# Performance work log

Measured on AMD Instinct MI355X. Metric: run time of the kernel, lower is better.

Reference implementation:

```python
import jax, jax.numpy as jnp
import numpy as np

B, S, H = 8, 512, 768
NH, DH = 12, 64
I = 3072
E = 8
TOPK = 2
EPS = 1e-12


def _ln(x, g, b):
    m = jnp.mean(x, axis=-1, keepdims=True)
    v = jnp.mean(jnp.square(x - m), axis=-1, keepdims=True)
    return (x - m) * jax.lax.rsqrt(v + EPS) * g + b


def setup_inputs() -> dict:
    key = jax.random.key(0)
    ks = jax.random.split(key, 20)
    s_h = 1.0 / np.sqrt(H)
    s_i = 1.0 / np.sqrt(I)
    inp = {
        "hidden_states": jax.random.normal(ks[0], (B, S, H), jnp.float32),
        "Wq": jax.random.normal(ks[1], (H, H), jnp.float32) * s_h,
        "bq": jnp.zeros((H,), jnp.float32),
        "Wk": jax.random.normal(ks[2], (H, H), jnp.float32) * s_h,
        "bk": jnp.zeros((H,), jnp.float32),
        "Wv": jax.random.normal(ks[3], (H, H), jnp.float32) * s_h,
        "bv": jnp.zeros((H,), jnp.float32),
        "Wo": jax.random.normal(ks[4], (H, H), jnp.float32) * s_h,
        "bo": jnp.zeros((H,), jnp.float32),
        "ln_attn_g": jnp.ones((H,), jnp.float32),
        "ln_attn_b": jnp.zeros((H,), jnp.float32),
        "ln_ffn_g": jnp.ones((H,), jnp.float32),
        "ln_ffn_b": jnp.zeros((H,), jnp.float32),
        "Wr": jax.random.normal(ks[5], (H, E), jnp.float32) * s_h,
        "br": jnp.zeros((E,), jnp.float32),
        "W_up": jax.random.normal(ks[6], (E, H, I), jnp.float32) * s_h,
        "b_up": jnp.zeros((E, I), jnp.float32),
        "W_new": jax.random.normal(ks[7], (E, H, I), jnp.float32) * s_h,
        "b_new": jnp.zeros((E, I), jnp.float32),
        "W_down": jax.random.normal(ks[8], (E, I, H), jnp.float32) * s_i,
        "b_down": jnp.zeros((E, H), jnp.float32),
    }
    return inp


def reference(hidden_states, Wq, bq, Wk, bk, Wv, bv, Wo, bo,
              ln_attn_g, ln_attn_b, ln_ffn_g, ln_ffn_b,
              Wr, br, W_up, b_up, W_new, b_new, W_down, b_down):
    x = hidden_states
    # --- BertSelfAttention ---
    q = (x @ Wq + bq).reshape(B, S, NH, DH).transpose(0, 2, 1, 3)
    k = (x @ Wk + bk).reshape(B, S, NH, DH).transpose(0, 2, 1, 3)
    v = (x @ Wv + bv).reshape(B, S, NH, DH).transpose(0, 2, 1, 3)
    scores = jnp.einsum("bhqd,bhkd->bhqk", q, k) / np.sqrt(DH)
    probs = jax.nn.softmax(scores, axis=-1)
    ctx = jnp.einsum("bhqk,bhkd->bhqd", probs, v)
    ctx = ctx.transpose(0, 2, 1, 3).reshape(B, S, H)
    # --- BertSelfOutput: dense + residual + LayerNorm ---
    attention_output = _ln(ctx @ Wo + bo + x, ln_attn_g, ln_attn_b)
    # --- feed_forward_chunk: LayerNorm then token top-k MoE ---
    xl = _ln(attention_output, ln_ffn_g, ln_ffn_b)
    router_logits = xl @ Wr + br                      # [B,S,E]
    router_probs = jax.nn.softmax(router_logits, axis=-1)
    topw, topi = jax.lax.top_k(router_probs, TOPK)    # [B,S,K]
    topw = topw / jnp.sum(topw, axis=-1, keepdims=True)
    gates = jnp.sum(jax.nn.one_hot(topi, E, dtype=xl.dtype) * topw[..., None], axis=-2)  # [B,S,E]
    # --- experts (BertExpert: gelu(up(x)) * new(x) -> down), dense over E ---
    up = jax.nn.gelu(jnp.einsum("bsh,ehi->ebsi", xl, W_up) + b_up[:, None, None, :], approximate=False)
    gate_h = jnp.einsum("bsh,ehi->ebsi", xl, W_new) + b_new[:, None, None, :]
    y = jnp.einsum("ebsi,eih->ebsh", up * gate_h, W_down) + b_down[:, None, None, :]
    moe_out = jnp.einsum("ebsh,bse->bsh", y, gates)
    layer_output = moe_out + attention_output
    return layer_output, router_logits
```

## Files before the change

kernel.cpp:

```cpp
#include <hip/hip_runtime.h>
#include <hip/hip_bf16.h>
#include <cmath>


constexpr int cB = 8, cS = 512, cH = 768, cNH = 12, cDH = 64, cI = 3072, cE = 8;
constexpr int cT = cB * cS;
constexpr size_t TH = (size_t)cT * cH;

typedef __hip_bfloat16 bf16;
typedef __attribute__((ext_vector_type(8))) short s8v;
typedef __attribute__((ext_vector_type(4))) float f4v;

constexpr size_t SZ_WEXP     = (size_t)cE * cI * cH / 2;
constexpr size_t OFF_WUP_T   = 0;
constexpr size_t OFF_WNEW_T  = OFF_WUP_T + SZ_WEXP;
constexpr size_t OFF_WDOWN_T = OFF_WNEW_T + SZ_WEXP;
constexpr size_t OFF_QKV     = OFF_WDOWN_T + SZ_WEXP;
constexpr size_t OFF_CTX     = OFF_QKV + 4 * TH;
constexpr size_t OFF_XLB     = OFF_CTX + TH;
constexpr size_t OFF_WGT     = OFF_XLB + TH / 2;
constexpr size_t OFF_COUNTS  = OFF_WGT + 2 * cT;
constexpr size_t OFF_LISTS   = OFF_COUNTS + 16;

__device__ __forceinline__ void glds16(const void* g, void* l) {
    __builtin_amdgcn_global_load_lds(
        (const __attribute__((address_space(1))) unsigned int*)g,
        (__attribute__((address_space(3))) unsigned int*)l, 16, 0, 0);
}

__global__ void init_counts_kernel(int* __restrict__ counts) {
    if (threadIdx.x < cE) counts[threadIdx.x] = 0;
}

__global__ __launch_bounds__(256) void transpose_bf16_kernel(
    const float* __restrict__ src, bf16* __restrict__ dst, int R, int C) {
    __shared__ float tile[64][65];
    const size_t zb = (size_t)blockIdx.z * R * C;
    const int r0 = blockIdx.y * 64, c0 = blockIdx.x * 64;
    const int t = threadIdx.x;
    const int lr = t >> 4, lc = (t & 15) * 4;
#pragma unroll
    for (int i = 0; i < 4; ++i) {
        float4 v = *(const float4*)(src + zb + (size_t)(r0 + lr + i * 16) * C + c0 + lc);
        tile[lr + i * 16][lc + 0] = v.x; tile[lr + i * 16][lc + 1] = v.y;
        tile[lr + i * 16][lc + 2] = v.z; tile[lr + i * 16][lc + 3] = v.w;
    }
    __syncthreads();
#pragma unroll
    for (int i = 0; i < 4; ++i) {
        int cr = lr + i * 16;
        bf16 o[4];
#pragma unroll
        for (int j = 0; j < 4; ++j) o[j] = (bf16)tile[lc + j][cr];
        *(uint2*)(dst + zb + (size_t)(c0 + cr) * R + r0 + lc) = *(uint2*)o;
    }
}

__device__ __forceinline__ void gemm_body128(
    const float* __restrict__ A, const float* __restrict__ B,
    const float* __restrict__ bias, float* __restrict__ C,
    int N, int K, int m0, int n0, int kbeg, int kend, bool addb) {
    __shared__ float As[16 * 132];
    __shared__ float Bs[16 * 128];
    const int t = threadIdx.x;
    const int tx = t & 15, ty = t >> 4;
    const int ar = t >> 2, ac = (t & 3) * 4;
    const float* gB0 = B + (size_t)(kbeg + (t >> 5)) * N + n0 + (t & 31) * 4;
    float* dB0 = Bs + t * 4;
    float acc[8][8] = {};
    for (int k0 = kbeg; k0 < kend; k0 += 16) {
        float4 a0 = *(const float4*)(A + (size_t)(m0 + ar) * K + k0 + ac);
        float4 a1 = *(const float4*)(A + (size_t)(m0 + ar + 64) * K + k0 + ac);
        glds16(gB0, dB0);
        glds16(gB0 + (size_t)8 * N, dB0 + 1024);
        As[(ac + 0) * 132 + ar] = a0.x; As[(ac + 1) * 132 + ar] = a0.y;
        As[(ac + 2) * 132 + ar] = a0.z; As[(ac + 3) * 132 + ar] = a0.w;
        As[(ac + 0) * 132 + ar + 64] = a1.x; As[(ac + 1) * 132 + ar + 64] = a1.y;
        As[(ac + 2) * 132 + ar + 64] = a1.z; As[(ac + 3) * 132 + ar + 64] = a1.w;
        __syncthreads();
#pragma unroll
        for (int kk = 0; kk < 16; ++kk) {
            float a[8], b[8];
            *(float4*)&a[0] = *(const float4*)&As[kk * 132 + ty * 8];
            *(float4*)&a[4] = *(const float4*)&As[kk * 132 + ty * 8 + 4];
            *(float4*)&b[0] = *(const float4*)&Bs[kk * 128 + tx * 4];
            *(float4*)&b[4] = *(const float4*)&Bs[kk * 128 + tx * 4 + 64];
#pragma unroll
            for (int i = 0; i < 8; ++i)
#pragma unroll
                for (int j = 0; j < 8; ++j) acc[i][j] += a[i] * b[j];
        }
        __syncthreads();
        gB0 += (size_t)16 * N;
    }
#pragma unroll
    for (int i = 0; i < 8; ++i) {
        int m = m0 + ty * 8 + i;
        float4 o0, o1;
        o0.x = acc[i][0]; o0.y = acc[i][1]; o0.z = acc[i][2]; o0.w = acc[i][3];
        o1.x = acc[i][4]; o1.y = acc[i][5]; o1.z = acc[i][6]; o1.w = acc[i][7];
        if (addb) {
            o0.x += bias[n0 + tx * 4 + 0]; o0.y += bias[n0 + tx * 4 + 1];
            o0.z += bias[n0 + tx * 4 + 2]; o0.w += bias[n0 + tx * 4 + 3];
            o1.x += bias[n0 + 64 + tx * 4 + 0]; o1.y += bias[n0 + 64 + tx * 4 + 1];
            o1.z += bias[n0 + 64 + tx * 4 + 2]; o1.w += bias[n0 + 64 + tx * 4 + 3];
        }
        *(float4*)(C + (size_t)m * N + n0 + tx * 4) = o0;
        *(float4*)(C + (size_t)m * N + n0 + 64 + tx * 4) = o1;
    }
}

__global__ __launch_bounds__(256) void gemm_qkv_kernel(
    const float* __restrict__ A,
    const float* __restrict__ Wq, const float* __restrict__ Wk,
    const float* __restrict__ Wv,
    const float* __restrict__ bq, const float* __restrict__ bk,
    const float* __restrict__ bv,
    float* __restrict__ q0, float* __restrict__ k0, float* __restrict__ v0,
    float* __restrict__ q1, float* __restrict__ k1, float* __restrict__ v1) {
    const int z = blockIdx.z;
    const int p = z >> 1, ks = z & 1;
    const float* B = (p == 0) ? Wq : (p == 1) ? Wk : Wv;
    const float* bias = (p == 0) ? bq : (p == 1) ? bk : bv;
    float* C = (p == 0) ? (ks ? q1 : q0)
             : (p == 1) ? (ks ? k1 : k0)
                        : (ks ? v1 : v0);
    gemm_body128(A, B, bias, C, cH, cH, blockIdx.y * 128, blockIdx.x * 128,
                 ks * 384, ks * 384 + 384, ks == 0);
}

__global__ __launch_bounds__(256) void reduce_qkv_kernel(
    float* __restrict__ dst2, const float* __restrict__ src2,
    float* __restrict__ v0, const float* __restrict__ v1) {
    const size_t n2 = 2 * TH / 4, n3 = 3 * TH / 4;
    for (size_t i = (size_t)blockIdx.x * 256 + threadIdx.x; i < n3;
         i += (size_t)gridDim.x * 256) {
        if (i < n2) {
            float4 a = ((const float4*)dst2)[i];
            float4 b = ((const float4*)src2)[i];
            a.x += b.x; a.y += b.y; a.z += b.z; a.w += b.w;
            ((float4*)dst2)[i] = a;
        } else {
            size_t j = i - n2;
            float4 a = ((const float4*)v0)[j];
            float4 b = ((const float4*)v1)[j];
            a.x += b.x; a.y += b.y; a.z += b.z; a.w += b.w;
            ((float4*)v0)[j] = a;
        }
    }
}

__global__ __launch_bounds__(256) void gemm_wo_kernel(
    const float* __restrict__ A, const float* __restrict__ W,
    const float* __restrict__ bias,
    float* __restrict__ p0, float* __restrict__ p1,
    float* __restrict__ p2, float* __restrict__ p3) {
    const int ks = blockIdx.z;
    float* C = (ks == 0) ? p0 : (ks == 1) ? p1 : (ks == 2) ? p2 : p3;
    gemm_body128(A, W, bias, C, cH, cH, blockIdx.y * 128, blockIdx.x * 128,
                 ks * 192, ks * 192 + 192, ks == 0);
}

__global__ __launch_bounds__(256) void attn_kernel(
    const float* __restrict__ q, const float* __restrict__ k,
    const float* __restrict__ v, float* __restrict__ ctx) {
    __shared__ float sQ[64][68];
    __shared__ float sKV[64][68];
    __shared__ float sS[64][68];
    __shared__ float sM[64], sL[64], sAl[64];
    const int q0 = blockIdx.x * 64, h = blockIdx.y, b = blockIdx.z;
    const int t = threadIdx.x;
    const int lr = t >> 2, lq = (t & 3) * 16;
    {
        const float* gq = q + (size_t)(b * cS + q0 + lr) * cH + h * cDH + lq;
#pragma unroll
        for (int j = 0; j < 4; ++j) {
            float4 x = *(const float4*)(gq + j * 4);
            x.x *= 0.125f; x.y *= 0.125f; x.z *= 0.125f; x.w *= 0.125f;
            *(float4*)&sQ[lr][lq + j * 4] = x;
        }
    }
    if (t < 64) { sM[t] = -1e30f; sL[t] = 0.f; }
    const int c0 = t & 15, rr = (t >> 4) * 4;
    const int d4 = (t & 15) * 4, rp = (t >> 4) * 4;
    const int sr = t >> 2, sc = (t & 3) * 16;
    float4 o_acc[4];
#pragma unroll
    for (int i = 0; i < 4; ++i) o_acc[i] = make_float4(0.f, 0.f, 0.f, 0.f);

    for (int kt = 0; kt < 8; ++kt) {
        float4 kreg[4];
        {
            const float* gk = k + (size_t)(b * cS + kt * 64 + lr) * cH + h * cDH + lq;
#pragma unroll
            for (int j = 0; j < 4; ++j) kreg[j] = *(const float4*)(gk + j * 4);
        }
        __syncthreads();
#pragma unroll
        for (int j = 0; j < 4; ++j) *(float4*)&sKV[lr][lq + j * 4] = kreg[j];
        __syncthreads();
        float accS[4][4] = {};
#pragma unroll
        for (int d = 0; d < 64; d += 4) {
            float4 qv[4], kv[4];
#pragma unroll
            for (int i = 0; i < 4; ++i) qv[i] = *(const float4*)&sQ[rr + i][d];
#pragma unroll
            for (int j = 0; j < 4; ++j) kv[j] = *(const float4*)&sKV[c0 + 16 * j][d];
#pragma unroll
            for (int i = 0; i < 4; ++i)
#pragma unroll
                for (int j = 0; j < 4; ++j)
                    accS[i][j] += qv[i].x * kv[j].x + qv[i].y * kv[j].y +
                                  qv[i].z * kv[j].z + qv[i].w * kv[j].w;
        }
#pragma unroll
        for (int i = 0; i < 4; ++i)
#pragma unroll
            for (int j = 0; j < 4; ++j) sS[rr + i][c0 + 16 * j] = accS[i][j];
        float4 vreg[4];
        {
            const float* gv = v + (size_t)(b * cS + kt * 64 + lr) * cH + h * cDH + lq;
#pragma unroll
            for (int j = 0; j < 4; ++j) vreg[j] = *(const float4*)(gv + j * 4);
        }
        __syncthreads();
        {
            float4 s[4];
#pragma unroll
            for (int j = 0; j < 4; ++j) s[j] = *(const float4*)&sS[sr][sc + j * 4];
            float m = -1e30f;
#pragma unroll
            for (int j = 0; j < 4; ++j)
                m = fmaxf(m, fmaxf(fmaxf(s[j].x, s[j].y), fmaxf(s[j].z, s[j].w)));
            m = fmaxf(m, __shfl_xor(m, 1));
            m = fmaxf(m, __shfl_xor(m, 2));
            float m_old = sM[sr];
            float m_new = fmaxf(m_old, m);
            float sum = 0.f;
#pragma unroll
            for (int j = 0; j < 4; ++j) {
                s[j].x = __expf(s[j].x - m_new); s[j].y = __expf(s[j].y - m_new);
                s[j].z = __expf(s[j].z - m_new); s[j].w = __expf(s[j].w - m_new);
                sum += s[j].x + s[j].y + s[j].z + s[j].w;
                *(float4*)&sS[sr][sc + j * 4] = s[j];
            }
            sum += __shfl_xor(sum, 1);
            sum += __shfl_xor(sum, 2);
            if ((t & 3) == 0) {
                float alpha = __expf(m_old - m_new);
                sAl[sr] = alpha;
                sM[sr] = m_new;
                sL[sr] = sL[sr] * alpha + sum;
            }
        }
#pragma unroll
        for (int j = 0; j < 4; ++j) *(float4*)&sKV[lr][lq + j * 4] = vreg[j];
        __syncthreads();
#pragma unroll
        for (int i = 0; i < 4; ++i) {
            float al = sAl[rp + i];
            o_acc[i].x *= al; o_acc[i].y *= al; o_acc[i].z *= al; o_acc[i].w *= al;
        }
        for (int kk4 = 0; kk4 < 64; kk4 += 4) {
            float4 pv[4], vv[4];
#pragma unroll
            for (int i = 0; i < 4; ++i) pv[i] = *(const float4*)&sS[rp + i][kk4];
#pragma unroll
            for (int j = 0; j < 4; ++j) vv[j] = *(const float4*)&sKV[kk4 + j][d4];
#pragma unroll
            for (int i = 0; i < 4; ++i) {
                o_acc[i].x += pv[i].x * vv[0].x + pv[i].y * vv[1].x +
                              pv[i].z * vv[2].x + pv[i].w * vv[3].x;
                o_acc[i].y += pv[i].x * vv[0].y + pv[i].y * vv[1].y +
                              pv[i].z * vv[2].y + pv[i].w * vv[3].y;
                o_acc[i].z += pv[i].x * vv[0].z + pv[i].y * vv[1].z +
                              pv[i].z * vv[2].z + pv[i].w * vv[3].z;
                o_acc[i].w += pv[i].x * vv[0].w + pv[i].y * vv[1].w +
                              pv[i].z * vv[2].w + pv[i].w * vv[3].w;
            }
        }
    }
    __syncthreads();
#pragma unroll
    for (int i = 0; i < 4; ++i) {
        float inv = 1.0f / sL[rp + i];
        float4 o = o_acc[i];
        o.x *= inv; o.y *= inv; o.z *= inv; o.w *= inv;
        *(float4*)(ctx + (size_t)(b * cS + q0 + rp + i) * cH + h * cDH + d4) = o;
    }
}

__device__ __forceinline__ float block_reduce_sum(float v, float* red) {
#pragma unroll
    for (int o = 32; o; o >>= 1) v += __shfl_xor(v, o);
    __syncthreads();
    if ((threadIdx.x & 63) == 0) red[threadIdx.x >> 6] = v;
    __syncthreads();
    return red[0] + red[1] + red[2] + red[3];
}

__global__ __launch_bounds__(256) void ln_router_kernel(
    const float* __restrict__ dense0, const float* __restrict__ dense1,
    const float* __restrict__ dense2, const float* __restrict__ dense3,
    const float* __restrict__ resid,
    const float* __restrict__ g1, const float* __restrict__ b1,
    const float* __restrict__ g2, const float* __restrict__ b2,
    const float* __restrict__ Wr, const float* __restrict__ br,
    float* __restrict__ out, bf16* __restrict__ xlb,
    float* __restrict__ out_logits, float* __restrict__ wgt,
    int* __restrict__ counts, int* __restrict__ lists) {
    __shared__ float red[4];
    __shared__ float lred[4][8];
    const int t = blockIdx.x, tid = threadIdx.x;
    const size_t base = (size_t)t * cH;
    float v[3], s = 0.f;
#pragma unroll
    for (int i = 0; i < 3; ++i) {
        size_t ix = base + tid + 256 * i;
        v[i] = dense0[ix] + dense1[ix] + dense2[ix] + dense3[ix] + resid[ix];
        s += v[i];
    }
    const float mean = block_reduce_sum(s, red) * (1.0f / cH);
    float vs = 0.f;
#pragma unroll
    for (int i = 0; i < 3; ++i) { float d = v[i] - mean; vs += d * d; }
    const float rstd = rsqrtf(block_reduce_sum(vs, red) * (1.0f / cH) + 1e-12f);
    float a[3], s2 = 0.f;
#pragma unroll
    for (int i = 0; i < 3; ++i) {
        a[i] = (v[i] - mean) * rstd * g1[tid + 256 * i] + b1[tid + 256 * i];
        out[base + tid + 256 * i] = a[i];
        s2 += a[i];
    }
    const float mean2 = block_reduce_sum(s2, red) * (1.0f / cH);
    float vs2 = 0.f;
#pragma unroll
    for (int i = 0; i < 3; ++i) { float d = a[i] - mean2; vs2 += d * d; }
    const float rstd2 = rsqrtf(block_reduce_sum(vs2, red) * (1.0f / cH) + 1e-12f);
    float xl[3];
#pragma unroll
    for (int i = 0; i < 3; ++i) {
        xl[i] = (a[i] - mean2) * rstd2 * g2[tid + 256 * i] + b2[tid + 256 * i];
        xlb[base + tid + 256 * i] = (bf16)xl[i];
    }
    float lg[cE] = {};
#pragma unroll
    for (int i = 0; i < 3; ++i) {
        const float* wr = Wr + (size_t)(tid + 256 * i) * cE;
#pragma unroll
        for (int e = 0; e < cE; ++e) lg[e] += xl[i] * wr[e];
    }
#pragma unroll
    for (int e = 0; e < cE; ++e)
#pragma unroll
        for (int o = 32; o; o >>= 1) lg[e] += __shfl_xor(lg[e], o);
    if ((tid & 63) == 0)
#pragma unroll
        for (int e = 0; e < cE; ++e) lred[tid >> 6][e] = lg[e];
    __syncthreads();
    if (tid == 0) {
        float logits[cE];
#pragma unroll
        for (int e = 0; e < cE; ++e) {
            logits[e] = lred[0][e] + lred[1][e] + lred[2][e] + lred[3][e] + br[e];
            out_logits[(size_t)t * cE + e] = logits[e];
        }
        int i0 = 0;
        for (int e = 1; e < cE; ++e) if (logits[e] > logits[i0]) i0 = e;
        int i1 = (i0 == 0) ? 1 : 0;
        for (int e = 0; e < cE; ++e)
            if (e != i0 && logits[e] > logits[i1]) i1 = e;
        float e1 = __expf(logits[i1] - logits[i0]);
        float w0 = 1.0f / (1.0f + e1);
        float w1 = e1 * w0;
        wgt[t * 2 + 0] = w0;
        wgt[t * 2 + 1] = w1;
        int p0 = atomicAdd(&counts[i0], 1);
        lists[i0 * cT + p0] = t * 2 + 0;
        int p1 = atomicAdd(&counts[i1], 1);
        lists[i1 * cT + p1] = t * 2 + 1;
    }
}

__global__ __launch_bounds__(256) void expert_up_mfma_kernel(
    const bf16* __restrict__ xlb,
    const bf16* __restrict__ WupT, const bf16* __restrict__ WnewT,
    const float* __restrict__ b_up, const float* __restrict__ b_new,
    const int* __restrict__ counts, const int* __restrict__ lists,
    bf16* __restrict__ act) {
    const int e = blockIdx.z;
    const int cnt = counts[e];
    const int m0 = blockIdx.y * 128;
    if (m0 >= cnt) return;
    const int n0 = blockIdx.x * 64;
    __shared__ short sA[128 * 32], sB1[64 * 32], sB2[64 * 32];
    __shared__ int rowa[128];
    const int t = threadIdx.x;
    if (t < 128) {
        int idx = m0 + t;
        rowa[t] = (idx < cnt) ? lists[e * cT + idx] : -1;
    }
    __syncthreads();
    const int lane = t & 63, w = t >> 6;
    const int wm = (w >> 1) * 64, wn = (w & 1) * 32;
    const int rA0 = t >> 2, kc8 = (t & 3) * 8;
    int a0 = rowa[rA0], a1 = rowa[rA0 + 64];
    const bf16* gA0 = xlb + (size_t)(a0 < 0 ? 0 : (a0 >> 1)) * cH + kc8;
    const bf16* gA1 = xlb + (size_t)(a1 < 0 ? 0 : (a1 >> 1)) * cH + kc8;
    const bf16* B1 = WupT + (size_t)e * cI * cH;
    const bf16* B2 = WnewT + (size_t)e * cI * cH;
    const bf16* gB1 = B1 + (size_t)(n0 + rA0) * cH + kc8;
    const bf16* gB2 = B2 + (size_t)(n0 + rA0) * cH + kc8;
    short* dA0 = sA + t * 8;   short* dA1 = sA + (t + 256) * 8;
    short* dB1 = sB1 + t * 8;  short* dB2 = sB2 + t * 8;
    f4v zero = {0.f, 0.f, 0.f, 0.f};
    f4v acc1[4][2], acc2[4][2];
#pragma unroll
    for (int i = 0; i < 4; ++i)
#pragma unroll
        for (int j = 0; j < 2; ++j) { acc1[i][j] = zero; acc2[i][j] = zero; }
    const int fr = lane & 15, kg = (lane >> 4) * 8;
    for (int kk = 0; kk < cH; kk += 32) {
        glds16(gA0, dA0); glds16(gA1, dA1);
        glds16(gB1, dB1); glds16(gB2, dB2);
        __syncthreads();
        s8v af[4], bf1[2], bf2[2];
#pragma unroll
        for (int i = 0; i < 4; ++i)
            af[i] = *(const s8v*)(sA + (wm + i * 16 + fr) * 32 + kg);
#pragma unroll
        for (int j = 0; j < 2; ++j) {
            bf1[j] = *(const s8v*)(sB1 + (wn + j * 16 + fr) * 32 + kg);
            bf2[j] = *(const s8v*)(sB2 + (wn + j * 16 + fr) * 32 + kg);
        }
#pragma unroll
        for (int mi = 0; mi < 4; ++mi)
#pragma unroll
            for (int ni = 0; ni < 2; ++ni) {
                acc1[mi][ni] = __builtin_amdgcn_mfma_f32_16x16x32_bf16(
                    af[mi], bf1[ni], acc1[mi][ni], 0, 0, 0);
                acc2[mi][ni] = __builtin_amdgcn_mfma_f32_16x16x32_bf16(
                    af[mi], bf2[ni], acc2[mi][ni], 0, 0, 0);
            }
        __syncthreads();
        gA0 += 32; gA1 += 32; gB1 += 32; gB2 += 32;
    }
    const int cn = lane & 15, rq = (lane >> 4) * 4;
#pragma unroll
    for (int mi = 0; mi < 4; ++mi)
#pragma unroll
        for (int r = 0; r < 4; ++r) {
            int ml = wm + mi * 16 + rq + r;
            int a = rowa[ml];
            if (a < 0) continue;
            bf16* orow = act + (size_t)a * cI + n0 + wn;
#pragma unroll
            for (int ni = 0; ni < 2; ++ni) {
                int nl = ni * 16 + cn;
                float up = acc1[mi][ni][r] + b_up[e * cI + n0 + wn + nl];
                float nw = acc2[mi][ni][r] + b_new[e * cI + n0 + wn + nl];
                float g = 0.5f * up * (1.0f + erff(up * 0.70710678118654752f));
                orow[nl] = (bf16)(g * nw);
            }
        }
}

__global__ __launch_bounds__(256) void expert_down_mfma_kernel(
    const bf16* __restrict__ act, const bf16* __restrict__ WdownT,
    const float* __restrict__ b_down,
    const int* __restrict__ counts, const int* __restrict__ lists,
    const float* __restrict__ wgt, float* __restrict__ out) {
    const int e = blockIdx.z;
    const int cnt = counts[e];
    const int m0 = blockIdx.y * 128;
    if (m0 >= cnt) return;
    const int n0 = blockIdx.x * 128;
    __shared__ short sA[128 * 32], sB[128 * 32];
    __shared__ int rowa[128];
    const int t = threadIdx.x;
    if (t < 128) {
        int idx = m0 + t;
        rowa[t] = (idx < cnt) ? lists[e * cT + idx] : -1;
    }
    __syncthreads();
    const int lane = t & 63, w = t >> 6;
    const int wm = (w >> 1) * 64, wn = (w & 1) * 64;
    const int rA0 = t >> 2, kc8 = (t & 3) * 8;
    int a0 = rowa[rA0], a1 = rowa[rA0 + 64];
    const bf16* gA0 = act + (size_t)(a0 < 0 ? 0 : a0) * cI + kc8;
    const bf16* gA1 = act + (size_t)(a1 < 0 ? 0 : a1) * cI + kc8;
    const bf16* BT = WdownT + (size_t)e * cH * cI;
    const bf16* gB0 = BT + (size_t)(n0 + rA0) * cI + kc8;
    const bf16* gB1 = BT + (size_t)(n0 + rA0 + 64) * cI + kc8;
    short* dA0 = sA + t * 8;       short* dA1 = sA + (t + 256) * 8;
    short* dB0 = sB + t * 8;       short* dB1 = sB + (t + 256) * 8;
    f4v zero = {0.f, 0.f, 0.f, 0.f};
    f4v acc[4][4];
#pragma unroll
    for (int i = 0; i < 4; ++i)
#pragma unroll
        for (int j = 0; j < 4; ++j) acc[i][j] = zero;
    const int fr = lane & 15, kg = (lane >> 4) * 8;
    for (int kk = 0; kk < cI; kk += 32) {
        glds16(gA0, dA0); glds16(gA1, dA1);
        glds16(gB0, dB0); glds16(gB1, dB1);
        __syncthreads();
        s8v af[4], bf[4];
#pragma unroll
        for (int i = 0; i < 4; ++i) af[i] = *(const s8v*)(sA + (wm + i * 16 + fr) * 32 + kg);
#pragma unroll
        for (int i = 0; i < 4; ++i) bf[i] = *(const s8v*)(sB + (wn + i * 16 + fr) * 32 + kg);
#pragma unroll
        for (int mi = 0; mi < 4; ++mi)
#pragma unroll
            for (int ni = 0; ni < 4; ++ni)
                acc[mi][ni] = __builtin_amdgcn_mfma_f32_16x16x32_bf16(
                    af[mi], bf[ni], acc[mi][ni], 0, 0, 0);
        __syncthreads();
        gA0 += 32; gA1 += 32; gB0 += 32; gB1 += 32;
    }
    const int cn = lane & 15, rq = (lane >> 4) * 4;
#pragma unroll
    for (int mi = 0; mi < 4; ++mi)
#pragma unroll
        for (int r = 0; r < 4; ++r) {
            int ml = wm + mi * 16 + rq + r;
            int a = rowa[ml];
            if (a < 0) continue;
            int token = a >> 1;
            float wv = wgt[a];
#pragma unroll
            for (int ni = 0; ni < 4; ++ni) {
                int n = n0 + wn + ni * 16 + cn;
                atomicAdd(&out[(size_t)token * cH + n],
                          wv * (acc[mi][ni][r] + b_down[e * cH + n]));
            }
        }
}

extern "C" void kernel_launch(void* const* d_in, const int* in_sizes, int n_in,
                              void* d_out, int out_size, void* d_ws, size_t ws_size,
                              hipStream_t stream) {
    const float* x      = (const float*)d_in[0];
    const float* Wq     = (const float*)d_in[1];
    const float* bq     = (const float*)d_in[2];
    const float* Wk     = (const float*)d_in[3];
    const float* bk     = (const float*)d_in[4];
    const float* Wv     = (const float*)d_in[5];
    const float* bv     = (const float*)d_in[6];
    const float* Wo     = (const float*)d_in[7];
    const float* bo     = (const float*)d_in[8];
    const float* ln1g   = (const float*)d_in[9];
    const float* ln1b   = (const float*)d_in[10];
    const float* ln2g   = (const float*)d_in[11];
    const float* ln2b   = (const float*)d_in[12];
    const float* Wr     = (const float*)d_in[13];
    const float* br     = (const float*)d_in[14];
    const float* W_up   = (const float*)d_in[15];
    const float* b_up   = (const float*)d_in[16];
    const float* W_new  = (const float*)d_in[17];
    const float* b_new  = (const float*)d_in[18];
    const float* W_down = (const float*)d_in[19];
    const float* b_down = (const float*)d_in[20];

    float* out = (float*)d_out;
    float* ws  = (float*)d_ws;

    bf16* WupT   = (bf16*)(ws + OFF_WUP_T);
    bf16* WnewT  = (bf16*)(ws + OFF_WNEW_T);
    bf16* WdownT = (bf16*)(ws + OFF_WDOWN_T);
    float* q     = ws + OFF_QKV;
    float* k     = ws + OFF_QKV + TH;
    float* v     = ws + OFF_QKV + 2 * TH;
    float* tmp   = ws + OFF_QKV + 3 * TH;
    bf16* act    = (bf16*)(ws + OFF_QKV);
    float* ctx   = ws + OFF_CTX;
    bf16* xlb    = (bf16*)(ws + OFF_XLB);
    float* wgt   = ws + OFF_WGT;
    int* counts  = (int*)(ws + OFF_COUNTS);
    int* lists   = (int*)(ws + OFF_LISTS);

    init_counts_kernel<<<1, 64, 0, stream>>>(counts);

    transpose_bf16_kernel<<<dim3(48, 12, cE), 256, 0, stream>>>(W_up, WupT, cH, cI);
    transpose_bf16_kernel<<<dim3(48, 12, cE), 256, 0, stream>>>(W_new, WnewT, cH, cI);
    transpose_bf16_kernel<<<dim3(12, 48, cE), 256, 0, stream>>>(W_down, WdownT, cI, cH);

    gemm_qkv_kernel<<<dim3(cH / 128, cT / 128, 6), 256, 0, stream>>>(
        x, Wq, Wk, Wv, bq, bk, bv, q, k, v, tmp, ctx, out);
    reduce_qkv_kernel<<<2048, 256, 0, stream>>>(q, tmp, v, out);
    attn_kernel<<<dim3(cS / 64, cNH, cB), 256, 0, stream>>>(q, k, v, ctx);
    gemm_wo_kernel<<<dim3(cH / 128, cT / 128, 4), 256, 0, stream>>>(
        ctx, Wo, bo, q, k, v, tmp);
    ln_router_kernel<<<cT, 256, 0, stream>>>(
        q, k, v, tmp, x, ln1g, ln1b, ln2g, ln2b, Wr, br,
        out, xlb, out + TH, wgt, counts, lists);

    expert_up_mfma_kernel<<<dim3(cI / 64, cT / 128, cE), 256, 0, stream>>>(
        xlb, WupT, WnewT, b_up, b_new, counts, lists, act);
    expert_down_mfma_kernel<<<dim3(cH / 128, cT / 128, cE), 256, 0, stream>>>(
        act, WdownT, b_down, counts, lists, wgt, out);
}
```

Measured before the change: 1.051 ms.

## Restructure fp32 QKV/Wo GEMMs to 32x256 tiles with direct-global A reads and XCD-aware mapping

Replaces the 128x128 shared-memory-tiled fp32 GEMM body with a 32x256 tile. Each wave handles 8 rows and reads its A rows straight from global memory as wave-uniform loads, and only B is staged in LDS. Block indices are remapped so consecutive row tiles land on the same XCD, which should improve L2 reuse of A and B. The smaller per-thread accumulator tile (8x4) lowers register pressure, but it also lowers arithmetic intensity per LDS load and leans on cache hits for the A reads.

```diff
diff --git a/kernel.cpp b/kernel.cpp
--- a/kernel.cpp
+++ b/kernel.cpp
@@ -56,57 +56,59 @@
     }
 }
 
-__device__ __forceinline__ void gemm_body128(
+__device__ __forceinline__ void gemm_body_sg(
     const float* __restrict__ A, const float* __restrict__ B,
     const float* __restrict__ bias, float* __restrict__ C,
     int N, int K, int m0, int n0, int kbeg, int kend, bool addb) {
-    __shared__ float As[16 * 132];
-    __shared__ float Bs[16 * 128];
+    __shared__ float Bs[16 * 256];
     const int t = threadIdx.x;
-    const int tx = t & 15, ty = t >> 4;
-    const int ar = t >> 2, ac = (t & 3) * 4;
-    const float* gB0 = B + (size_t)(kbeg + (t >> 5)) * N + n0 + (t & 31) * 4;
-    float* dB0 = Bs + t * 4;
-    float acc[8][8] = {};
+    const int wv = t >> 6, l = t & 63;
+    const int wu = __builtin_amdgcn_readfirstlane(wv);
+    const float* Ab = A + (size_t)(m0 + wu * 8) * K;
+    const float* gB = B + (size_t)(kbeg + wv * 4) * N + n0 + l * 4;
+    float* dB = Bs + (wv * 4) * 256 + l * 4;
+    float acc[8][4] = {};
     for (int k0 = kbeg; k0 < kend; k0 += 16) {
-        float4 a0 = *(const float4*)(A + (size_t)(m0 + ar) * K + k0 + ac);
-        float4 a1 = *(const float4*)(A + (size_t)(m0 + ar + 64) * K + k0 + ac);
-        glds16(gB0, dB0);
-        glds16(gB0 + (size_t)8 * N, dB0 + 1024);
-        As[(ac + 0) * 132 + ar] = a0.x; As[(ac + 1) * 132 + ar] = a0.y;
-        As[(ac + 2) * 132 + ar] = a0.z; As[(ac + 3) * 132 + ar] = a0.w;
-        As[(ac + 0) * 132 + ar + 64] = a1.x; As[(ac + 1) * 132 + ar + 64] = a1.y;
-        As[(ac + 2) * 132 + ar + 64] = a1.z; As[(ac + 3) * 132 + ar + 64] = a1.w;
-        __syncthreads();
-#pragma unroll
-        for (int kk = 0; kk < 16; ++kk) {
-            float a[8], b[8];
-            *(float4*)&a[0] = *(const float4*)&As[kk * 132 + ty * 8];
-            *(float4*)&a[4] = *(const float4*)&As[kk * 132 + ty * 8 + 4];
-            *(float4*)&b[0] = *(const float4*)&Bs[kk * 128 + tx * 4];
-            *(float4*)&b[4] = *(const float4*)&Bs[kk * 128 + tx * 4 + 64];
-#pragma unroll
-            for (int i = 0; i < 8; ++i)
-#pragma unroll
-                for (int j = 0; j < 8; ++j) acc[i][j] += a[i] * b[j];
-        }
-        __syncthreads();
-        gB0 += (size_t)16 * N;
-    }
-#pragma unroll
-    for (int i = 0; i < 8; ++i) {
-        int m = m0 + ty * 8 + i;
-        float4 o0, o1;
-        o0.x = acc[i][0]; o0.y = acc[i][1]; o0.z = acc[i][2]; o0.w = acc[i][3];
-        o1.x = acc[i][4]; o1.y = acc[i][5]; o1.z = acc[i][6]; o1.w = acc[i][7];
+        glds16(gB, dB);
+        glds16(gB + (size_t)N, dB + 256);
+        glds16(gB + (size_t)2 * N, dB + 512);
+        glds16(gB + (size_t)3 * N, dB + 768);
+        __syncthreads();
+#pragma unroll
+        for (int q = 0; q < 4; ++q) {
+            float4 a4[8];
+#pragma unroll
+            for (int r = 0; r < 8; ++r)
+                a4[r] = *(const float4*)(Ab + (size_t)r * K + k0 + q * 4);
+#pragma unroll
+            for (int kq = 0; kq < 4; ++kq) {
+                float4 b = *(const float4*)&Bs[(q * 4 + kq) * 256 + l * 4];
+#pragma unroll
+                for (int r = 0; r < 8; ++r) {
+                    float av = (kq == 0) ? a4[r].x : (kq == 1) ? a4[r].y
+                             : (kq == 2) ? a4[r].z : a4[r].w;
+                    acc[r][0] += av * b.x;
+                    acc[r][1] += av * b.y;
+                    acc[r][2] += av * b.z;
+                    acc[r][3] += av * b.w;
+                }
+            }
+        }
+        __syncthreads();
+        gB += (size_t)16 * N;
+    }
+#pragma unroll
+    for (int r = 0; r < 8; ++r) {
+        int m = m0 + wu * 8 + r;
+        float4 o;
+        o.x = acc[r][0]; o.y = acc[r][1]; o.z = acc[r][2]; o.w = acc[r][3];
         if (addb) {
-            o0.x += bias[n0 + tx * 4 + 0]; o0.y += bias[n0 + tx * 4 + 1];
-            o0.z += bias[n0 + tx * 4 + 2]; o0.w += bias[n0 + tx * 4 + 3];
-            o1.x += bias[n0 + 64 + tx * 4 + 0]; o1.y += bias[n0 + 64 + tx * 4 + 1];
-            o1.z += bias[n0 + 64 + tx * 4 + 2]; o1.w += bias[n0 + 64 + tx * 4 + 3];
-        }
-        *(float4*)(C + (size_t)m * N + n0 + tx * 4) = o0;
-        *(float4*)(C + (size_t)m * N + n0 + 64 + tx * 4) = o1;
+            o.x += bias[n0 + l * 4 + 0];
+            o.y += bias[n0 + l * 4 + 1];
+            o.z += bias[n0 + l * 4 + 2];
+            o.w += bias[n0 + l * 4 + 3];
+        }
+        *(float4*)(C + (size_t)m * N + n0 + l * 4) = o;
     }
 }
 
@@ -118,14 +120,19 @@
     const float* __restrict__ bv,
     float* __restrict__ q0, float* __restrict__ k0, float* __restrict__ v0,
     float* __restrict__ q1, float* __restrict__ k1, float* __restrict__ v1) {
-    const int z = blockIdx.z;
-    const int p = z >> 1, ks = z & 1;
-    const float* B = (p == 0) ? Wq : (p == 1) ? Wk : Wv;
-    const float* bias = (p == 0) ? bq : (p == 1) ? bk : bv;
-    float* C = (p == 0) ? (ks ? q1 : q0)
-             : (p == 1) ? (ks ? k1 : k0)
-                        : (ks ? v1 : v0);
-    gemm_body128(A, B, bias, C, cH, cH, blockIdx.y * 128, blockIdx.x * 128,
+    const int f = blockIdx.x + 3 * blockIdx.y + 384 * blockIdx.z;
+    const int xcd = f & 7, p = f >> 3;
+    const int yl = p & 15;
+    const int n  = (p >> 4) % 3;
+    const int pz = p / 48;
+    const int y  = xcd * 16 + yl;
+    const int proj = pz >> 1, ks = pz & 1;
+    const float* B = (proj == 0) ? Wq : (proj == 1) ? Wk : Wv;
+    const float* bias = (proj == 0) ? bq : (proj == 1) ? bk : bv;
+    float* C = (proj == 0) ? (ks ? q1 : q0)
+             : (proj == 1) ? (ks ? k1 : k0)
+                           : (ks ? v1 : v0);
+    gemm_body_sg(A, B, bias, C, cH, cH, y * 32, n * 256,
                  ks * 384, ks * 384 + 384, ks == 0);
 }
 
@@ -155,9 +162,14 @@
     const float* __restrict__ bias,
     float* __restrict__ p0, float* __restrict__ p1,
     float* __restrict__ p2, float* __restrict__ p3) {
-    const int ks = blockIdx.z;
+    const int f = blockIdx.x + 3 * blockIdx.y + 384 * blockIdx.z;
+    const int xcd = f & 7, p = f >> 3;
+    const int yl = p & 15;
+    const int n  = (p >> 4) % 3;
+    const int ks = p / 48;
+    const int y  = xcd * 16 + yl;
     float* C = (ks == 0) ? p0 : (ks == 1) ? p1 : (ks == 2) ? p2 : p3;
-    gemm_body128(A, W, bias, C, cH, cH, blockIdx.y * 128, blockIdx.x * 128,
+    gemm_body_sg(A, W, bias, C, cH, cH, y * 32, n * 256,
                  ks * 192, ks * 192 + 192, ks == 0);
 }
 
@@ -587,11 +599,11 @@
     transpose_bf16_kernel<<<dim3(48, 12, cE), 256, 0, stream>>>(W_new, WnewT, cH, cI);
     transpose_bf16_kernel<<<dim3(12, 48, cE), 256, 0, stream>>>(W_down, WdownT, cI, cH);
 
-    gemm_qkv_kernel<<<dim3(cH / 128, cT / 128, 6), 256, 0, stream>>>(
+    gemm_qkv_kernel<<<dim3(3, 128, 6), 256, 0, stream>>>(
         x, Wq, Wk, Wv, bq, bk, bv, q, k, v, tmp, ctx, out);
     reduce_qkv_kernel<<<2048, 256, 0, stream>>>(q, tmp, v, out);
     attn_kernel<<<dim3(cS / 64, cNH, cB), 256, 0, stream>>>(q, k, v, ctx);
-    gemm_wo_kernel<<<dim3(cH / 128, cT / 128, 4), 256, 0, stream>>>(
+    gemm_wo_kernel<<<dim3(3, 128, 4), 256, 0, stream>>>(
         ctx, Wo, bo, q, k, v, tmp);
     ln_router_kernel<<<cT, 256, 0, stream>>>(
         q, k, v, tmp, x, ln1g, ln1b, ln2g, ln2b, Wr, br,
```

New measurement: 1.046 ms. About the same (-0.5%).
